# Kernel optimization log

Measured on AMD Instinct MI355X. Metric: run time of the kernel, lower is better.

## Reference

```python
import jax, jax.numpy as jnp
import numpy as np

BS, NA, NE, NAL = 128, 16, 16, 15
OWN, ALD, END = 30, 10, 10
H, HD, HYP, NACT = 64, 4, 64, 22
OUT_E = ((END + 1) * H + 1) * HD  # hyper_enemy output dim (weights + unused bias part)
OUT_A = ALD * H * HD


def setup_inputs() -> dict:
    key = jax.random.key(0)
    ks = jax.random.split(key, 30)
    s = 0.05
    r = lambda i, shape: jax.random.normal(ks[i], shape, dtype=jnp.float32) * s
    return {
        'bs': BS,
        'own_feats': r(0, (BS * NA, OWN)),
        'ally_feats': r(1, (BS * NA * NAL, ALD)),
        'enemy_feats': r(2, (BS * NA * NE, END)),
        'hidden_state': r(3, (BS * NA, H)),
        'fc1_w': r(4, (OWN, H)), 'fc1_b': r(5, (H,)),
        'he_w1': r(6, (END, HYP)), 'he_b1': r(7, (HYP,)),
        'he_w2': r(8, (HYP, OUT_E)), 'he_b2': r(9, (OUT_E,)),
        'ha_w1': r(10, (ALD, HYP)), 'ha_b1': r(11, (HYP,)),
        'ha_w2': r(12, (HYP, OUT_A)), 'ha_b2': r(13, (OUT_A,)),
        'merger_w': jnp.ones((1, HD, H), dtype=jnp.float32),
        'gru_wih': r(14, (3 * H, H)), 'gru_whh': r(15, (3 * H, H)),
        'gru_bih': r(16, (3 * H,)), 'gru_bhh': r(17, (3 * H,)),
        'fc2_w1': r(18, (H, H)), 'fc2_b1': r(19, (H,)),
        'fc2_w2': r(20, (H, NACT - 3)), 'fc2_b2': r(21, (NACT - 3,)),
        'pass_w1': r(22, (H, H)), 'pass_b1': r(23, (H,)),
        'pass_w2': r(24, (H, 3)), 'pass_b2': r(25, (3,)),
    }


def reference(bs, own_feats, ally_feats, enemy_feats, hidden_state,
              fc1_w, fc1_b, he_w1, he_b1, he_w2, he_b2,
              ha_w1, ha_b1, ha_w2, ha_b2, merger_w,
              gru_wih, gru_whh, gru_bih, gru_bhh,
              fc2_w1, fc2_b1, fc2_w2, fc2_b2,
              pass_w1, pass_b1, pass_w2, pass_b2):
    # own embedding: [bs*NA, H]
    emb_own = own_feats @ fc1_w + fc1_b

    # hypernet-generated enemy weights, consumed once then summed over enemies
    he = jax.nn.relu(enemy_feats @ he_w1 + he_b1) @ he_w2 + he_b2  # [bs*NA*NE, OUT_E]
    w_en = he[:, :END * H * HD].reshape(-1, END, H * HD)
    emb_en = jnp.einsum('ri,rio->ro', enemy_feats, w_en)
    emb_en = emb_en.reshape(bs * NA, NE, HD, H).sum(axis=1)  # [bs*NA, HD, H]

    ha = jax.nn.relu(ally_feats @ ha_w1 + ha_b1) @ ha_w2 + ha_b2  # [bs*NA*NAL, OUT_A]
    w_al = ha.reshape(-1, ALD, H * HD)
    emb_al4 = jnp.einsum('ri,rio->ro', ally_feats, w_al).reshape(bs * NA, NAL, HD, H)

    # passing_mlp -> [bs*NA, NAL, HD, 3]; permute/mean over heads, max over allies
    p = jax.nn.relu(emb_al4 @ pass_w1 + pass_b1) @ pass_w2 + pass_b2
    passing_dim = jnp.transpose(p, (0, 1, 3, 2)).mean(axis=-1)  # [bs*NA, NAL, 3]
    passing_embed = passing_dim.max(axis=1)  # [bs*NA, 3]

    emb_al = emb_al4.sum(axis=1)  # [bs*NA, HD, H]

    # Merger over heads
    mw = jax.nn.softmax(merger_w, axis=1)  # [1, HD, H]
    merged = jnp.sum(mw * (emb_en + emb_al), axis=1)  # [bs*NA, H]

    x = jax.nn.relu(emb_own + merged)

    # GRUCell (torch gate order: r, z, n)
    h_in = hidden_state.reshape(-1, H)
    gi = x @ gru_wih.T + gru_bih
    gh = h_in @ gru_whh.T + gru_bhh
    ir, iz, inn = jnp.split(gi, 3, axis=-1)
    hr, hz, hn = jnp.split(gh, 3, axis=-1)
    rg = jax.nn.sigmoid(ir + hr)
    zg = jax.nn.sigmoid(iz + hz)
    ng = jnp.tanh(inn + rg * hn)
    hh = (1.0 - zg) * ng + zg * h_in

    q_normal = (jax.nn.relu(hh @ fc2_w1 + fc2_b1) @ fc2_w2 + fc2_b2).reshape(bs, NA, -1)
    pe = passing_embed.reshape(bs, NA, 3)
    q = jnp.concatenate([q_normal[:, :, :9], pe, q_normal[:, :, 9:]], axis=-1)
    return q.reshape(bs, NA, -1), hh.reshape(bs, NA, -1)
```

## Files before the change

### kernel.cpp

```cpp
#include <hip/hip_runtime.h>
#include <hip/hip_bf16.h>

#define RAG   2048
#define KP2   704
#define QOFF  45056

typedef __attribute__((ext_vector_type(8))) short short8;
typedef __attribute__((ext_vector_type(4))) float f32x4;

__device__ inline unsigned short f2bf(float f){
    unsigned u = __float_as_uint(f);
    u += 0x7fffu + ((u >> 16) & 1u);
    return (unsigned short)(u >> 16);
}
__device__ inline unsigned pack2(float a, float b){
    return (unsigned)f2bf(a) | ((unsigned)f2bf(b) << 16);
}
__device__ inline void gload_lds(const void* g, void* l){
    __builtin_amdgcn_global_load_lds(
        (const __attribute__((address_space(1))) void*)g,
        (__attribute__((address_space(3))) void*)l, 16, 0, 0);
}

__global__ void __launch_bounds__(256) k_usum(
    const float* __restrict__ ef, const float* __restrict__ hew1, const float* __restrict__ heb1,
    const float* __restrict__ af, const float* __restrict__ haw1, const float* __restrict__ hab1,
    const float* __restrict__ hew2, const float* __restrict__ heb2,
    const float* __restrict__ haw2, const float* __restrict__ hab2,
    const float* __restrict__ wih, const float* __restrict__ whh, const float* __restrict__ f2w1,
    unsigned short* __restrict__ Bte, unsigned short* __restrict__ Bta,
    unsigned short* __restrict__ Wgru, unsigned short* __restrict__ B2,
    unsigned short* __restrict__ ha1, unsigned short* __restrict__ usum)
{
    int bb = blockIdx.x, tid = threadIdx.x;
    if (bb >= RAG){
        int p = bb - RAG;
        if (p < 22){
            int mat = p & 1;
            int s   = p >> 1;
            const float* w2 = mat ? haw2 : hew2;
            const float* b2 = mat ? hab2 : heb2;
            int ld = mat ? 2560 : 2820;
            unsigned short* Bt = mat ? Bta : Bte;
            int n = tid, n7 = n & 7;
            unsigned pk[32];
#pragma unroll
            for (int u2 = 0; u2 < 32; ++u2){
                int cst = u2 >> 2;
                int co  = cst ^ n7;
                int j0  = (u2 * 2) & 7;
                int k0 = s*64 + co*8 + j0, k1 = k0 + 1;
                float v0 = 0.f, v1 = 0.f;
                if (k0 < 640)      v0 = w2[(k0 & 63)*ld + (k0 >> 6)*256 + n];
                else if (k0 < 650) v0 = b2[(k0 - 640)*256 + n];
                if (k1 < 640)      v1 = w2[(k1 & 63)*ld + (k1 >> 6)*256 + n];
                else if (k1 < 650) v1 = b2[(k1 - 640)*256 + n];
                pk[u2] = pack2(v0, v1);
            }
            uint4* dst = (uint4*)&Bt[s*16384 + n*64];
#pragma unroll
            for (int q = 0; q < 8; ++q)
                dst[q] = (uint4){pk[q*4], pk[q*4+1], pk[q*4+2], pk[q*4+3]};
        } else if (p < 38){
            int base = (p - 22) * 2048;
#pragma unroll
            for (int i = 0; i < 8; ++i){
                int it = base + i*256 + tid;
                int n = it >> 7, k = it & 127;
                float v;
                if (n < 128)      v = (k < 64) ? wih[n*64 + k] : whh[n*64 + k - 64];
                else if (n < 192) v = (k < 64) ? wih[n*64 + k] : 0.f;
                else              v = (k < 64) ? 0.f : whh[(n-64)*64 + k - 64];
                Wgru[it] = f2bf(v);
            }
        } else {
            int base = (p - 38) * 2048;
#pragma unroll
            for (int i = 0; i < 8; ++i){
                int it = base + i*256 + tid;
                int n = it >> 6, k = it & 63;
                B2[it] = f2bf(f2w1[k*64 + n]);
            }
        }
        return;
    }
    __shared__ float s_ef[16][10], s_af[15][10];
    __shared__ float s_he[16][64], s_ha[15][64];
    int ag = bb;
    if (tid < 160) s_ef[tid/10][tid%10] = ef[ag*160 + tid];
    if (tid < 150) s_af[tid/10][tid%10] = af[ag*150 + tid];
    __syncthreads();
    for (int idx = tid; idx < 16*64; idx += 256){
        int en = idx >> 6, h = idx & 63;
        float s = heb1[h];
#pragma unroll
        for (int i = 0; i < 10; ++i) s = fmaf(s_ef[en][i], hew1[i*64 + h], s);
        s_he[en][h] = fmaxf(s, 0.f);
    }
    for (int idx = tid; idx < 15*64; idx += 256){
        int l = idx >> 6, h = idx & 63;
        float s = hab1[h];
#pragma unroll
        for (int i = 0; i < 10; ++i) s = fmaf(s_af[l][i], haw1[i*64 + h], s);
        s_ha[l][h] = fmaxf(s, 0.f);
    }
    __syncthreads();
    for (int idx = tid; idx < 15*64; idx += 256){
        int l = idx >> 6, h = idx & 63;
        ha1[(ag*15 + l)*64 + h] = f2bf(s_ha[l][h]);
    }
    for (int k = tid; k < KP2; k += 256){
        float ue = 0.f, ua = 0.f;
        if (k < 640){
            int i = k >> 6, h = k & 63;
#pragma unroll
            for (int en = 0; en < 16; ++en) ue = fmaf(s_he[en][h], s_ef[en][i], ue);
#pragma unroll
            for (int l = 0; l < 15; ++l) ua = fmaf(s_ha[l][h], s_af[l][i], ua);
        } else if (k < 650){
            int i = k - 640;
#pragma unroll
            for (int en = 0; en < 16; ++en) ue += s_ef[en][i];
#pragma unroll
            for (int l = 0; l < 15; ++l) ua += s_af[l][i];
        }
        usum[ag*KP2 + k]         = f2bf(ue);
        usum[(RAG + ag)*KP2 + k] = f2bf(ua);
    }
}

#define MFMA_STEP()                                                              \
    _Pragma("unroll")                                                            \
    for (int kk = 0; kk < 2; ++kk){                                              \
        int ch = ((kk*4 + quad) ^ l7) * 8;                                       \
        short8 a_[4], b_[4];                                                     \
        _Pragma("unroll")                                                        \
        for (int mt = 0; mt < 4; ++mt) a_[mt] = *(const short8*)&sA[(mt*16 + l15)*64 + ch]; \
        _Pragma("unroll")                                                        \
        for (int nt = 0; nt < 4; ++nt) b_[nt] = *(const short8*)&sB[(w*64 + nt*16 + l15)*64 + ch]; \
        _Pragma("unroll")                                                        \
        for (int mt = 0; mt < 4; ++mt)                                           \
        _Pragma("unroll")                                                        \
        for (int nt = 0; nt < 4; ++nt)                                           \
            acc[mt][nt] = __builtin_amdgcn_mfma_f32_16x16x32_bf16(a_[mt], b_[nt], acc[mt][nt], 0, 0, 0); \
    }

__global__ void __launch_bounds__(256, 2) k_gemm(
    const unsigned short* __restrict__ Bte, const unsigned short* __restrict__ Bta,
    const unsigned short* __restrict__ ha1, const float* __restrict__ af,
    const unsigned short* __restrict__ usum,
    const float* __restrict__ pw1, const float* __restrict__ pb1,
    const float* __restrict__ pw2, const float* __restrict__ pb2,
    float* __restrict__ emb, float* __restrict__ p2)
{
    __shared__ __align__(16) char smem[50176];
    unsigned short* sB  = (unsigned short*)smem;
    unsigned short* sA  = (unsigned short*)(smem + 32768);
    unsigned short* sW1 = (unsigned short*)(smem + 40960);

    int tid = threadIdx.x;
    int w = tid >> 6, lane = tid & 63;
    int l15 = lane & 15, quad = lane >> 4, l7 = l15 & 7;
    int bb = blockIdx.x;

    f32x4 acc[4][4];
#pragma unroll
    for (int a = 0; a < 4; ++a)
#pragma unroll
    for (int b = 0; b < 4; ++b) acc[a][b] = (f32x4){0.f, 0.f, 0.f, 0.f};

    if (bb < 480){
        int row0 = bb * 64;
        int r = tid >> 2, c4 = tid & 3, r7 = r & 7;
#pragma unroll
        for (int p = 0; p < 16; ++p){
            int idx = tid + p*256;
            sW1[(idx & 63)*72 + (idx >> 6)] = f2bf(pw1[idx]);
        }
        float af_reg[10];
        {
            const float* ap = af + (row0 + r)*10;
#pragma unroll
            for (int i = 0; i < 10; ++i) af_reg[i] = ap[i];
        }
        float h1f[16];
        {
            const unsigned short* hp = ha1 + (size_t)(row0 + r)*64 + c4*16;
            uint4 ra = *(const uint4*)hp;
            uint4 rb = *(const uint4*)(hp + 8);
            unsigned va[4] = {ra.x, ra.y, ra.z, ra.w};
            unsigned vb[4] = {rb.x, rb.y, rb.z, rb.w};
#pragma unroll
            for (int q = 0; q < 4; ++q){
                h1f[q*2+0]   = __uint_as_float(va[q] << 16);
                h1f[q*2+1]   = __uint_as_float(va[q] & 0xffff0000u);
                h1f[8+q*2+0] = __uint_as_float(vb[q] << 16);
                h1f[8+q*2+1] = __uint_as_float(vb[q] & 0xffff0000u);
            }
        }
        unsigned short* sAw0 = &sA[r*64 + (((2*c4)     ^ r7) * 8)];
        unsigned short* sAw1 = &sA[r*64 + (((2*c4 + 1) ^ r7) * 8)];
        const char* Bb = (const char*)Bta;
#pragma unroll
        for (int s = 0; s < 10; ++s){
            __syncthreads();
            const char* Bstep = Bb + s*32768;
#pragma unroll
            for (int ii = 0; ii < 8; ++ii)
                gload_lds(Bstep + w*8192 + ii*1024 + lane*16, smem + w*8192 + ii*1024);
            float avf = af_reg[s];
            uint4 p0, p1;
            p0.x = pack2(h1f[0]*avf,  h1f[1]*avf);  p0.y = pack2(h1f[2]*avf,  h1f[3]*avf);
            p0.z = pack2(h1f[4]*avf,  h1f[5]*avf);  p0.w = pack2(h1f[6]*avf,  h1f[7]*avf);
            p1.x = pack2(h1f[8]*avf,  h1f[9]*avf);  p1.y = pack2(h1f[10]*avf, h1f[11]*avf);
            p1.z = pack2(h1f[12]*avf, h1f[13]*avf); p1.w = pack2(h1f[14]*avf, h1f[15]*avf);
            *(uint4*)sAw0 = p0;
            *(uint4*)sAw1 = p1;
            __syncthreads();
            MFMA_STEP()
        }
        {
            __syncthreads();
            const char* Bstep = Bb + 10*32768;
#pragma unroll
            for (int ii = 0; ii < 8; ++ii)
                gload_lds(Bstep + w*8192 + ii*1024 + lane*16, smem + w*8192 + ii*1024);
            uint4 p0 = (uint4){0,0,0,0}, p1 = (uint4){0,0,0,0};
            if (c4 == 0){
                p0.x = pack2(af_reg[0], af_reg[1]); p0.y = pack2(af_reg[2], af_reg[3]);
                p0.z = pack2(af_reg[4], af_reg[5]); p0.w = pack2(af_reg[6], af_reg[7]);
                p1.x = pack2(af_reg[8], af_reg[9]);
            }
            *(uint4*)sAw0 = p0;
            *(uint4*)sAw1 = p1;
            __syncthreads();
            MFMA_STEP()
        }
        __syncthreads();
        unsigned short* sE = (unsigned short*)(smem + w*9216);
#pragma unroll
        for (int mt = 0; mt < 4; ++mt)
#pragma unroll
        for (int nt = 0; nt < 4; ++nt)
#pragma unroll
        for (int rg = 0; rg < 4; ++rg)
            sE[(mt*16 + quad*4 + rg)*72 + nt*16 + l15] = f2bf(acc[mt][nt][rg]);
        __syncthreads();
        f32x4 yacc[4][4];
#pragma unroll
        for (int a = 0; a < 4; ++a)
#pragma unroll
        for (int b = 0; b < 4; ++b) yacc[a][b] = (f32x4){0.f, 0.f, 0.f, 0.f};
#pragma unroll
        for (int kb = 0; kb < 2; ++kb){
            short8 ea[4], wb[4];
#pragma unroll
            for (int mt = 0; mt < 4; ++mt) ea[mt] = *(const short8*)&sE[(mt*16 + l15)*72 + kb*32 + quad*8];
#pragma unroll
            for (int ot = 0; ot < 4; ++ot) wb[ot] = *(const short8*)&sW1[(ot*16 + l15)*72 + kb*32 + quad*8];
#pragma unroll
            for (int mt = 0; mt < 4; ++mt)
#pragma unroll
            for (int ot = 0; ot < 4; ++ot)
                yacc[mt][ot] = __builtin_amdgcn_mfma_f32_16x16x32_bf16(ea[mt], wb[ot], yacc[mt][ot], 0, 0, 0);
        }
        float pb1v[4], w2r[4][3];
#pragma unroll
        for (int ot = 0; ot < 4; ++ot){
            pb1v[ot] = pb1[ot*16 + l15];
#pragma unroll
            for (int j = 0; j < 3; ++j) w2r[ot][j] = pw2[(ot*16 + l15)*3 + j];
        }
#pragma unroll
        for (int mt = 0; mt < 4; ++mt){
            float part[4][3];
#pragma unroll
            for (int rg = 0; rg < 4; ++rg)
#pragma unroll
            for (int j = 0; j < 3; ++j) part[rg][j] = 0.f;
#pragma unroll
            for (int ot = 0; ot < 4; ++ot)
#pragma unroll
            for (int rg = 0; rg < 4; ++rg){
                float yv = fmaxf(yacc[mt][ot][rg] + pb1v[ot], 0.f);
#pragma unroll
                for (int j = 0; j < 3; ++j) part[rg][j] = fmaf(yv, w2r[ot][j], part[rg][j]);
            }
#pragma unroll
            for (int off = 1; off < 16; off <<= 1)
#pragma unroll
            for (int rg = 0; rg < 4; ++rg)
#pragma unroll
            for (int j = 0; j < 3; ++j) part[rg][j] += __shfl_xor(part[rg][j], off, 64);
            if (l15 == 0){
#pragma unroll
                for (int rg = 0; rg < 4; ++rg)
#pragma unroll
                for (int j = 0; j < 3; ++j)
                    p2[(row0 + mt*16 + quad*4 + rg)*12 + w*3 + j] = part[rg][j] + pb2[j];
            }
        }
    } else {
        int row0 = (bb - 480) * 64;
        const char* Bb = (const char*)((row0 < RAG) ? Bte : Bta);
        const char* Ub = (const char*)usum;
        int corig = (lane & 7) ^ (lane >> 3);
        size_t aoff = (size_t)(row0 + w*16 + (lane >> 3)) * (KP2*2) + corig*16;
#pragma unroll
        for (int s = 0; s < 11; ++s){
            __syncthreads();
            const char* Bstep = Bb + s*32768;
#pragma unroll
            for (int ii = 0; ii < 8; ++ii)
                gload_lds(Bstep + w*8192 + ii*1024 + lane*16, smem + w*8192 + ii*1024);
            gload_lds(Ub + aoff + s*128,              smem + 32768 + w*2048);
            gload_lds(Ub + aoff + 8*(KP2*2) + s*128,  smem + 32768 + w*2048 + 1024);
            __syncthreads();
            MFMA_STEP()
        }
#pragma unroll
        for (int mt = 0; mt < 4; ++mt)
#pragma unroll
        for (int nt = 0; nt < 4; ++nt)
#pragma unroll
        for (int rg = 0; rg < 4; ++rg)
            emb[(row0 + mt*16 + quad*4 + rg)*256 + w*64 + nt*16 + l15] = acc[mt][nt][rg];
    }
}

__global__ void __launch_bounds__(256) k_final(
    const float* __restrict__ own, const float* __restrict__ hidden,
    const float* __restrict__ fc1w, const float* __restrict__ fc1b,
    const float* __restrict__ mergw,
    const float* __restrict__ bih, const float* __restrict__ bhh,
    const float* __restrict__ f2b1, const float* __restrict__ f2w2, const float* __restrict__ f2b2,
    const unsigned short* __restrict__ Wgru, const unsigned short* __restrict__ B2,
    const float* __restrict__ emb, const float* __restrict__ p2,
    float* __restrict__ out)
{
    __shared__ __align__(16) unsigned short sA16[16*128];
    __shared__ float sHin[16*65];
    __shared__ float sG[256*17];
    __shared__ float sH2f[16*65];
    __shared__ __align__(16) unsigned short sH2b[16*64];
    __shared__ float sY[16*68];

    int tid = threadIdx.x;
    int w = tid >> 6, lane = tid & 63;
    int l15 = lane & 15, quad = lane >> 4;
    int ag0 = blockIdx.x * 16;

#pragma unroll
    for (int p = 0; p < 4; ++p){
        int idx = tid + p*256;
        int h = idx & 63, a = idx >> 6;
        int ag = ag0 + a;
        float s = fc1b[h];
        const float* ow = own + ag*30;
#pragma unroll
        for (int c = 0; c < 30; ++c) s = fmaf(ow[c], fc1w[c*64 + h], s);
        float m0 = mergw[h], m1 = mergw[64+h], m2 = mergw[128+h], m3 = mergw[192+h];
        float mx = fmaxf(fmaxf(m0, m1), fmaxf(m2, m3));
        float e0 = __expf(m0-mx), e1 = __expf(m1-mx), e2 = __expf(m2-mx), e3 = __expf(m3-mx);
        float inv = 1.f / (e0+e1+e2+e3);
        const float* een = emb + ag*256;
        const float* eal = emb + (RAG + ag)*256;
        float mg = (e0*(een[h]+eal[h]) + e1*(een[64+h]+eal[64+h]) +
                    e2*(een[128+h]+eal[128+h]) + e3*(een[192+h]+eal[192+h])) * inv;
        float x = fmaxf(s + mg, 0.f);
        float hin = hidden[ag*64 + h];
        sA16[a*128 + h]      = f2bf(x);
        sA16[a*128 + 64 + h] = f2bf(hin);
        sHin[a*65 + h] = hin;
    }
    __syncthreads();
    {
        f32x4 g_[4];
#pragma unroll
        for (int t = 0; t < 4; ++t) g_[t] = (f32x4){0.f,0.f,0.f,0.f};
#pragma unroll
        for (int ks = 0; ks < 4; ++ks){
            int kt = ks*32;
            short8 a8 = *(const short8*)&sA16[l15*128 + kt + quad*8];
#pragma unroll
            for (int t = 0; t < 4; ++t){
                int col = (w*4 + t)*16 + l15;
                short8 b8 = *(const short8*)&Wgru[col*128 + kt + quad*8];
                g_[t] = __builtin_amdgcn_mfma_f32_16x16x32_bf16(a8, b8, g_[t], 0, 0, 0);
            }
        }
#pragma unroll
        for (int t = 0; t < 4; ++t){
            int col = (w*4 + t)*16 + l15;
#pragma unroll
            for (int rg = 0; rg < 4; ++rg) sG[col*17 + quad*4 + rg] = g_[t][rg];
        }
    }
    __syncthreads();
#pragma unroll
    for (int p = 0; p < 4; ++p){
        int idx = tid + p*256;
        int a = idx & 15, h = idx >> 4;
        float rs  = sG[h*17 + a]        + bih[h]      + bhh[h];
        float zs  = sG[(64+h)*17 + a]   + bih[64+h]   + bhh[64+h];
        float in_ = sG[(128+h)*17 + a]  + bih[128+h];
        float hn  = sG[(192+h)*17 + a]  + bhh[128+h];
        float r = 1.f / (1.f + __expf(-rs));
        float z = 1.f / (1.f + __expf(-zs));
        float n = tanhf(in_ + r*hn);
        float hv = (1.f - z)*n + z*sHin[a*65 + h];
        sH2f[a*65 + h] = hv;
        sH2b[a*64 + h] = f2bf(hv);
    }
    __syncthreads();
    {
        f32x4 y = (f32x4){0.f,0.f,0.f,0.f};
#pragma unroll
        for (int ks = 0; ks < 2; ++ks){
            int kt = ks*32;
            short8 a8 = *(const short8*)&sH2b[l15*64 + kt + quad*8];
            short8 b8 = *(const short8*)&B2[(w*16 + l15)*64 + kt + quad*8];
            y = __builtin_amdgcn_mfma_f32_16x16x32_bf16(a8, b8, y, 0, 0, 0);
        }
        float b1v = f2b1[w*16 + l15];
#pragma unroll
        for (int rg = 0; rg < 4; ++rg)
            sY[(quad*4 + rg)*68 + w*16 + l15] = fmaxf(y[rg] + b1v, 0.f);
    }
    __syncthreads();
    for (int idx = tid; idx < 16*19; idx += 256){
        int a = idx / 19, j = idx - a*19;
        float s2 = f2b2[j];
        for (int c = 0; c < 64; ++c) s2 = fmaf(sY[a*68 + c], f2w2[c*19 + j], s2);
        out[(ag0 + a)*22 + ((j < 9) ? j : j + 3)] = s2;
    }
    if (tid < 48){
        int a = tid / 3, j = tid - a*3;
        float best = -1e30f;
        const float* pp = p2 + (ag0 + a)*180;
        for (int l = 0; l < 15; ++l){
            float mean = 0.25f*(pp[l*12 + j] + pp[l*12 + 3 + j] + pp[l*12 + 6 + j] + pp[l*12 + 9 + j]);
            best = fmaxf(best, mean);
        }
        out[(ag0 + a)*22 + 9 + j] = best;
    }
#pragma unroll
    for (int p = 0; p < 4; ++p){
        int idx = tid + p*256;
        int h = idx & 63, a = idx >> 6;
        out[QOFF + (ag0 + a)*64 + h] = sH2f[a*65 + h];
    }
}

extern "C" void kernel_launch(void* const* d_in, const int* in_sizes, int n_in,
                              void* d_out, int out_size, void* d_ws, size_t ws_size,
                              hipStream_t stream) {
    const float* own    = (const float*)d_in[1];
    const float* allyf  = (const float*)d_in[2];
    const float* enemyf = (const float*)d_in[3];
    const float* hidden = (const float*)d_in[4];
    const float* fc1w   = (const float*)d_in[5];
    const float* fc1b   = (const float*)d_in[6];
    const float* hew1   = (const float*)d_in[7];
    const float* heb1   = (const float*)d_in[8];
    const float* hew2   = (const float*)d_in[9];
    const float* heb2   = (const float*)d_in[10];
    const float* haw1   = (const float*)d_in[11];
    const float* hab1   = (const float*)d_in[12];
    const float* haw2   = (const float*)d_in[13];
    const float* hab2   = (const float*)d_in[14];
    const float* mergw  = (const float*)d_in[15];
    const float* wih    = (const float*)d_in[16];
    const float* whh    = (const float*)d_in[17];
    const float* bih    = (const float*)d_in[18];
    const float* bhh    = (const float*)d_in[19];
    const float* f2w1   = (const float*)d_in[20];
    const float* f2b1   = (const float*)d_in[21];
    const float* f2w2   = (const float*)d_in[22];
    const float* f2b2   = (const float*)d_in[23];
    const float* pw1    = (const float*)d_in[24];
    const float* pb1    = (const float*)d_in[25];
    const float* pw2    = (const float*)d_in[26];
    const float* pb2    = (const float*)d_in[27];
    float* out = (float*)d_out;

    char* W = (char*)d_ws;
    unsigned short* Bte  = (unsigned short*)(W + 0);
    unsigned short* Bta  = (unsigned short*)(W + 360448);
    unsigned short* usum = (unsigned short*)(W + 720896);
    float*          emb  = (float*)(W + 6488064);
    float*          p2   = (float*)(W + 10682368);
    unsigned short* ha1  = (unsigned short*)(W + 12156928);
    unsigned short* Wgru = (unsigned short*)(W + 16089088);
    unsigned short* B2   = (unsigned short*)(W + 16154624);

    k_usum<<<RAG + 40, 256, 0, stream>>>(enemyf, hew1, heb1, allyf, haw1, hab1,
                                         hew2, heb2, haw2, hab2, wih, whh, f2w1,
                                         Bte, Bta, Wgru, B2, ha1, usum);
    k_gemm<<<544, 256, 0, stream>>>(Bte, Bta, ha1, allyf, usum,
                                    pw1, pb1, pw2, pb2, emb, p2);
    k_final<<<RAG/16, 256, 0, stream>>>(own, hidden, fc1w, fc1b, mergw,
                                        bih, bhh, f2b1, f2w2, f2b2,
                                        Wgru, B2, emb, p2, out);
}
```

Baseline: 187.3 us.

## Double GEMM row tile to 128 rows per block to reuse B tiles

```diff
diff --git a/kernel.cpp b/kernel.cpp
--- a/kernel.cpp
+++ b/kernel.cpp
@@ -129,17 +129,17 @@
     }
 }
 
-#define MFMA_STEP()                                                              \
+#define MFMA_STEP8()                                                             \
     _Pragma("unroll")                                                            \
     for (int kk = 0; kk < 2; ++kk){                                              \
         int ch = ((kk*4 + quad) ^ l7) * 8;                                       \
-        short8 a_[4], b_[4];                                                     \
+        short8 a_[8], b_[4];                                                     \
         _Pragma("unroll")                                                        \
-        for (int mt = 0; mt < 4; ++mt) a_[mt] = *(const short8*)&sA[(mt*16 + l15)*64 + ch]; \
+        for (int mt = 0; mt < 8; ++mt) a_[mt] = *(const short8*)&sA[(mt*16 + l15)*64 + ch]; \
         _Pragma("unroll")                                                        \
         for (int nt = 0; nt < 4; ++nt) b_[nt] = *(const short8*)&sB[(w*64 + nt*16 + l15)*64 + ch]; \
         _Pragma("unroll")                                                        \
-        for (int mt = 0; mt < 4; ++mt)                                           \
+        for (int mt = 0; mt < 8; ++mt)                                           \
         _Pragma("unroll")                                                        \
         for (int nt = 0; nt < 4; ++nt)                                           \
             acc[mt][nt] = __builtin_amdgcn_mfma_f32_16x16x32_bf16(a_[mt], b_[nt], acc[mt][nt], 0, 0, 0); \
@@ -153,25 +153,25 @@
     const float* __restrict__ pw2, const float* __restrict__ pb2,
     float* __restrict__ emb, float* __restrict__ p2)
 {
-    __shared__ __align__(16) char smem[50176];
+    __shared__ __align__(16) char smem[58368];
     unsigned short* sB  = (unsigned short*)smem;
     unsigned short* sA  = (unsigned short*)(smem + 32768);
-    unsigned short* sW1 = (unsigned short*)(smem + 40960);
+    unsigned short* sW1 = (unsigned short*)(smem + 49152);
 
     int tid = threadIdx.x;
     int w = tid >> 6, lane = tid & 63;
     int l15 = lane & 15, quad = lane >> 4, l7 = l15 & 7;
     int bb = blockIdx.x;
 
-    f32x4 acc[4][4];
-#pragma unroll
-    for (int a = 0; a < 4; ++a)
+    f32x4 acc[8][4];
+#pragma unroll
+    for (int a = 0; a < 8; ++a)
 #pragma unroll
     for (int b = 0; b < 4; ++b) acc[a][b] = (f32x4){0.f, 0.f, 0.f, 0.f};
 
-    if (bb < 480){
-        int row0 = bb * 64;
-        int r = tid >> 2, c4 = tid & 3, r7 = r & 7;
+    if (bb < 240){
+        int row0 = bb * 128;
+        int r = tid >> 1, half = tid & 1, r7 = r & 7;
 #pragma unroll
         for (int p = 0; p < 16; ++p){
             int idx = tid + p*256;
@@ -183,23 +183,24 @@
 #pragma unroll
             for (int i = 0; i < 10; ++i) af_reg[i] = ap[i];
         }
-        float h1f[16];
+        float h1f[32];
         {
-            const unsigned short* hp = ha1 + (size_t)(row0 + r)*64 + c4*16;
-            uint4 ra = *(const uint4*)hp;
-            uint4 rb = *(const uint4*)(hp + 8);
-            unsigned va[4] = {ra.x, ra.y, ra.z, ra.w};
-            unsigned vb[4] = {rb.x, rb.y, rb.z, rb.w};
-#pragma unroll
-            for (int q = 0; q < 4; ++q){
-                h1f[q*2+0]   = __uint_as_float(va[q] << 16);
-                h1f[q*2+1]   = __uint_as_float(va[q] & 0xffff0000u);
-                h1f[8+q*2+0] = __uint_as_float(vb[q] << 16);
-                h1f[8+q*2+1] = __uint_as_float(vb[q] & 0xffff0000u);
-            }
-        }
-        unsigned short* sAw0 = &sA[r*64 + (((2*c4)     ^ r7) * 8)];
-        unsigned short* sAw1 = &sA[r*64 + (((2*c4 + 1) ^ r7) * 8)];
+            const unsigned short* hp = ha1 + (size_t)(row0 + r)*64 + half*32;
+#pragma unroll
+            for (int m = 0; m < 4; ++m){
+                uint4 u = *(const uint4*)(hp + m*8);
+                unsigned uu[4] = {u.x, u.y, u.z, u.w};
+#pragma unroll
+                for (int q = 0; q < 4; ++q){
+                    h1f[m*8 + q*2 + 0] = __uint_as_float(uu[q] << 16);
+                    h1f[m*8 + q*2 + 1] = __uint_as_float(uu[q] & 0xffff0000u);
+                }
+            }
+        }
+        unsigned short* sAw[4];
+#pragma unroll
+        for (int q = 0; q < 4; ++q)
+            sAw[q] = &sA[r*64 + (((half*4 + q) ^ r7) * 8)];
         const char* Bb = (const char*)Bta;
 #pragma unroll
         for (int s = 0; s < 10; ++s){
@@ -209,15 +210,17 @@
             for (int ii = 0; ii < 8; ++ii)
                 gload_lds(Bstep + w*8192 + ii*1024 + lane*16, smem + w*8192 + ii*1024);
             float avf = af_reg[s];
-            uint4 p0, p1;
-            p0.x = pack2(h1f[0]*avf,  h1f[1]*avf);  p0.y = pack2(h1f[2]*avf,  h1f[3]*avf);
-            p0.z = pack2(h1f[4]*avf,  h1f[5]*avf);  p0.w = pack2(h1f[6]*avf,  h1f[7]*avf);
-            p1.x = pack2(h1f[8]*avf,  h1f[9]*avf);  p1.y = pack2(h1f[10]*avf, h1f[11]*avf);
-            p1.z = pack2(h1f[12]*avf, h1f[13]*avf); p1.w = pack2(h1f[14]*avf, h1f[15]*avf);
-            *(uint4*)sAw0 = p0;
-            *(uint4*)sAw1 = p1;
-            __syncthreads();
-            MFMA_STEP()
+#pragma unroll
+            for (int q = 0; q < 4; ++q){
+                uint4 pv;
+                pv.x = pack2(h1f[q*8+0]*avf, h1f[q*8+1]*avf);
+                pv.y = pack2(h1f[q*8+2]*avf, h1f[q*8+3]*avf);
+                pv.z = pack2(h1f[q*8+4]*avf, h1f[q*8+5]*avf);
+                pv.w = pack2(h1f[q*8+6]*avf, h1f[q*8+7]*avf);
+                *(uint4*)sAw[q] = pv;
+            }
+            __syncthreads();
+            MFMA_STEP8()
         }
         {
             __syncthreads();
@@ -225,44 +228,18 @@
 #pragma unroll
             for (int ii = 0; ii < 8; ++ii)
                 gload_lds(Bstep + w*8192 + ii*1024 + lane*16, smem + w*8192 + ii*1024);
-            uint4 p0 = (uint4){0,0,0,0}, p1 = (uint4){0,0,0,0};
-            if (c4 == 0){
-                p0.x = pack2(af_reg[0], af_reg[1]); p0.y = pack2(af_reg[2], af_reg[3]);
-                p0.z = pack2(af_reg[4], af_reg[5]); p0.w = pack2(af_reg[6], af_reg[7]);
-                p1.x = pack2(af_reg[8], af_reg[9]);
-            }
-            *(uint4*)sAw0 = p0;
-            *(uint4*)sAw1 = p1;
-            __syncthreads();
-            MFMA_STEP()
-        }
-        __syncthreads();
-        unsigned short* sE = (unsigned short*)(smem + w*9216);
-#pragma unroll
-        for (int mt = 0; mt < 4; ++mt)
-#pragma unroll
-        for (int nt = 0; nt < 4; ++nt)
-#pragma unroll
-        for (int rg = 0; rg < 4; ++rg)
-            sE[(mt*16 + quad*4 + rg)*72 + nt*16 + l15] = f2bf(acc[mt][nt][rg]);
-        __syncthreads();
-        f32x4 yacc[4][4];
-#pragma unroll
-        for (int a = 0; a < 4; ++a)
-#pragma unroll
-        for (int b = 0; b < 4; ++b) yacc[a][b] = (f32x4){0.f, 0.f, 0.f, 0.f};
-#pragma unroll
-        for (int kb = 0; kb < 2; ++kb){
-            short8 ea[4], wb[4];
-#pragma unroll
-            for (int mt = 0; mt < 4; ++mt) ea[mt] = *(const short8*)&sE[(mt*16 + l15)*72 + kb*32 + quad*8];
-#pragma unroll
-            for (int ot = 0; ot < 4; ++ot) wb[ot] = *(const short8*)&sW1[(ot*16 + l15)*72 + kb*32 + quad*8];
-#pragma unroll
-            for (int mt = 0; mt < 4; ++mt)
-#pragma unroll
-            for (int ot = 0; ot < 4; ++ot)
-                yacc[mt][ot] = __builtin_amdgcn_mfma_f32_16x16x32_bf16(ea[mt], wb[ot], yacc[mt][ot], 0, 0, 0);
+            uint4 pv[4];
+#pragma unroll
+            for (int q = 0; q < 4; ++q) pv[q] = (uint4){0,0,0,0};
+            if (half == 0){
+                pv[0].x = pack2(af_reg[0], af_reg[1]); pv[0].y = pack2(af_reg[2], af_reg[3]);
+                pv[0].z = pack2(af_reg[4], af_reg[5]); pv[0].w = pack2(af_reg[6], af_reg[7]);
+                pv[1].x = pack2(af_reg[8], af_reg[9]);
+            }
+#pragma unroll
+            for (int q = 0; q < 4; ++q) *(uint4*)sAw[q] = pv[q];
+            __syncthreads();
+            MFMA_STEP8()
         }
         float pb1v[4], w2r[4][3];
 #pragma unroll
@@ -271,41 +248,72 @@
 #pragma unroll
             for (int j = 0; j < 3; ++j) w2r[ot][j] = pw2[(ot*16 + l15)*3 + j];
         }
-#pragma unroll
-        for (int mt = 0; mt < 4; ++mt){
-            float part[4][3];
+        unsigned short* sE = (unsigned short*)(smem + w*9216);
+#pragma unroll
+        for (int ps = 0; ps < 2; ++ps){
+            __syncthreads();
+#pragma unroll
+            for (int mt = 0; mt < 4; ++mt)
+#pragma unroll
+            for (int nt = 0; nt < 4; ++nt)
 #pragma unroll
             for (int rg = 0; rg < 4; ++rg)
-#pragma unroll
-            for (int j = 0; j < 3; ++j) part[rg][j] = 0.f;
-#pragma unroll
-            for (int ot = 0; ot < 4; ++ot)
-#pragma unroll
-            for (int rg = 0; rg < 4; ++rg){
-                float yv = fmaxf(yacc[mt][ot][rg] + pb1v[ot], 0.f);
-#pragma unroll
-                for (int j = 0; j < 3; ++j) part[rg][j] = fmaf(yv, w2r[ot][j], part[rg][j]);
-            }
-#pragma unroll
-            for (int off = 1; off < 16; off <<= 1)
-#pragma unroll
-            for (int rg = 0; rg < 4; ++rg)
-#pragma unroll
-            for (int j = 0; j < 3; ++j) part[rg][j] += __shfl_xor(part[rg][j], off, 64);
-            if (l15 == 0){
+                sE[(mt*16 + quad*4 + rg)*72 + nt*16 + l15] = f2bf(acc[ps*4 + mt][nt][rg]);
+            __syncthreads();
+            f32x4 yacc[4][4];
+#pragma unroll
+            for (int a = 0; a < 4; ++a)
+#pragma unroll
+            for (int b = 0; b < 4; ++b) yacc[a][b] = (f32x4){0.f, 0.f, 0.f, 0.f};
+#pragma unroll
+            for (int kb = 0; kb < 2; ++kb){
+                short8 ea[4], wb[4];
+#pragma unroll
+                for (int mt = 0; mt < 4; ++mt) ea[mt] = *(const short8*)&sE[(mt*16 + l15)*72 + kb*32 + quad*8];
+#pragma unroll
+                for (int ot = 0; ot < 4; ++ot) wb[ot] = *(const short8*)&sW1[(ot*16 + l15)*72 + kb*32 + quad*8];
+#pragma unroll
+                for (int mt = 0; mt < 4; ++mt)
+#pragma unroll
+                for (int ot = 0; ot < 4; ++ot)
+                    yacc[mt][ot] = __builtin_amdgcn_mfma_f32_16x16x32_bf16(ea[mt], wb[ot], yacc[mt][ot], 0, 0, 0);
+            }
+#pragma unroll
+            for (int mt = 0; mt < 4; ++mt){
+                float part[4][3];
 #pragma unroll
                 for (int rg = 0; rg < 4; ++rg)
 #pragma unroll
-                for (int j = 0; j < 3; ++j)
-                    p2[(row0 + mt*16 + quad*4 + rg)*12 + w*3 + j] = part[rg][j] + pb2[j];
+                for (int j = 0; j < 3; ++j) part[rg][j] = 0.f;
+#pragma unroll
+                for (int ot = 0; ot < 4; ++ot)
+#pragma unroll
+                for (int rg = 0; rg < 4; ++rg){
+                    float yv = fmaxf(yacc[mt][ot][rg] + pb1v[ot], 0.f);
+#pragma unroll
+                    for (int j = 0; j < 3; ++j) part[rg][j] = fmaf(yv, w2r[ot][j], part[rg][j]);
+                }
+#pragma unroll
+                for (int off = 1; off < 16; off <<= 1)
+#pragma unroll
+                for (int rg = 0; rg < 4; ++rg)
+#pragma unroll
+                for (int j = 0; j < 3; ++j) part[rg][j] += __shfl_xor(part[rg][j], off, 64);
+                if (l15 == 0){
+#pragma unroll
+                    for (int rg = 0; rg < 4; ++rg)
+#pragma unroll
+                    for (int j = 0; j < 3; ++j)
+                        p2[(row0 + ps*64 + mt*16 + quad*4 + rg)*12 + w*3 + j] = part[rg][j] + pb2[j];
+                }
             }
         }
     } else {
-        int row0 = (bb - 480) * 64;
+        int row0 = (bb - 240) * 128;
         const char* Bb = (const char*)((row0 < RAG) ? Bte : Bta);
         const char* Ub = (const char*)usum;
         int corig = (lane & 7) ^ (lane >> 3);
-        size_t aoff = (size_t)(row0 + w*16 + (lane >> 3)) * (KP2*2) + corig*16;
+        size_t abase = (size_t)(row0 + w*32 + (lane >> 3)) * (KP2*2) + corig*16;
 #pragma unroll
         for (int s = 0; s < 11; ++s){
             __syncthreads();
@@ -313,13 +321,15 @@
 #pragma unroll
             for (int ii = 0; ii < 8; ++ii)
                 gload_lds(Bstep + w*8192 + ii*1024 + lane*16, smem + w*8192 + ii*1024);
-            gload_lds(Ub + aoff + s*128,              smem + 32768 + w*2048);
-            gload_lds(Ub + aoff + 8*(KP2*2) + s*128,  smem + 32768 + w*2048 + 1024);
-            __syncthreads();
-            MFMA_STEP()
-        }
-#pragma unroll
-        for (int mt = 0; mt < 4; ++mt)
+#pragma unroll
+            for (int ii = 0; ii < 4; ++ii)
+                gload_lds(Ub + abase + (size_t)ii*8*(KP2*2) + s*128,
+                          smem + 32768 + w*4096 + ii*1024);
+            __syncthreads();
+            MFMA_STEP8()
+        }
+#pragma unroll
+        for (int mt = 0; mt < 8; ++mt)
 #pragma unroll
         for (int nt = 0; nt < 4; ++nt)
 #pragma unroll
@@ -497,7 +507,7 @@
     k_usum<<<RAG + 40, 256, 0, stream>>>(enemyf, hew1, heb1, allyf, haw1, hab1,
                                          hew2, heb2, haw2, hab2, wih, whh, f2w1,
                                          Bte, Bta, Wgru, B2, ha1, usum);
-    k_gemm<<<544, 256, 0, stream>>>(Bte, Bta, ha1, allyf, usum,
+    k_gemm<<<272, 256, 0, stream>>>(Bte, Bta, ha1, allyf, usum,
                                     pw1, pb1, pw2, pb2, emb, p2);
     k_final<<<RAG/16, 256, 0, stream>>>(own, hidden, fc1w, fc1b, mergw,
                                         bih, bhh, f2b1, f2w2, f2b2,
```

After: 189.0 us. About the same (+0.9%).

## Split k_gemm output columns across two blocks to double grid and occupancy

Applied to the files above, without the earlier changes.

```diff
diff --git a/kernel.cpp b/kernel.cpp
--- a/kernel.cpp
+++ b/kernel.cpp
@@ -129,23 +129,23 @@
     }
 }
 
-#define MFMA_STEP()                                                              \
+#define MFMA_STEP42()                                                            \
     _Pragma("unroll")                                                            \
     for (int kk = 0; kk < 2; ++kk){                                              \
         int ch = ((kk*4 + quad) ^ l7) * 8;                                       \
-        short8 a_[4], b_[4];                                                     \
+        short8 a_[4], b_[2];                                                     \
         _Pragma("unroll")                                                        \
         for (int mt = 0; mt < 4; ++mt) a_[mt] = *(const short8*)&sA[(mt*16 + l15)*64 + ch]; \
         _Pragma("unroll")                                                        \
-        for (int nt = 0; nt < 4; ++nt) b_[nt] = *(const short8*)&sB[(w*64 + nt*16 + l15)*64 + ch]; \
+        for (int nt = 0; nt < 2; ++nt) b_[nt] = *(const short8*)&sB[(w*32 + nt*16 + l15)*64 + ch]; \
         _Pragma("unroll")                                                        \
         for (int mt = 0; mt < 4; ++mt)                                           \
         _Pragma("unroll")                                                        \
-        for (int nt = 0; nt < 4; ++nt)                                           \
+        for (int nt = 0; nt < 2; ++nt)                                           \
             acc[mt][nt] = __builtin_amdgcn_mfma_f32_16x16x32_bf16(a_[mt], b_[nt], acc[mt][nt], 0, 0, 0); \
     }
 
-__global__ void __launch_bounds__(256, 2) k_gemm(
+__global__ void __launch_bounds__(256, 4) k_gemm(
     const unsigned short* __restrict__ Bte, const unsigned short* __restrict__ Bta,
     const unsigned short* __restrict__ ha1, const float* __restrict__ af,
     const unsigned short* __restrict__ usum,
@@ -153,30 +153,25 @@
     const float* __restrict__ pw2, const float* __restrict__ pb2,
     float* __restrict__ emb, float* __restrict__ p2)
 {
-    __shared__ __align__(16) char smem[50176];
-    unsigned short* sB  = (unsigned short*)smem;
-    unsigned short* sA  = (unsigned short*)(smem + 32768);
-    unsigned short* sW1 = (unsigned short*)(smem + 40960);
+    __shared__ __align__(16) char smem[33792];
+    unsigned short* sB = (unsigned short*)smem;
+    unsigned short* sA = (unsigned short*)(smem + 16384);
 
     int tid = threadIdx.x;
     int w = tid >> 6, lane = tid & 63;
     int l15 = lane & 15, quad = lane >> 4, l7 = l15 & 7;
     int bb = blockIdx.x;
 
-    f32x4 acc[4][4];
+    f32x4 acc[4][2];
 #pragma unroll
     for (int a = 0; a < 4; ++a)
 #pragma unroll
-    for (int b = 0; b < 4; ++b) acc[a][b] = (f32x4){0.f, 0.f, 0.f, 0.f};
-
-    if (bb < 480){
-        int row0 = bb * 64;
+    for (int b = 0; b < 2; ++b) acc[a][b] = (f32x4){0.f, 0.f, 0.f, 0.f};
+
+    if (bb < 960){
+        int rt = bb >> 1, c = bb & 1;
+        int row0 = rt * 64;
         int r = tid >> 2, c4 = tid & 3, r7 = r & 7;
-#pragma unroll
-        for (int p = 0; p < 16; ++p){
-            int idx = tid + p*256;
-            sW1[(idx & 63)*72 + (idx >> 6)] = f2bf(pw1[idx]);
-        }
         float af_reg[10];
         {
             const float* ap = af + (row0 + r)*10;
@@ -204,10 +199,10 @@
 #pragma unroll
         for (int s = 0; s < 10; ++s){
             __syncthreads();
-            const char* Bstep = Bb + s*32768;
-#pragma unroll
-            for (int ii = 0; ii < 8; ++ii)
-                gload_lds(Bstep + w*8192 + ii*1024 + lane*16, smem + w*8192 + ii*1024);
+            const char* Bstep = Bb + s*32768 + c*16384;
+#pragma unroll
+            for (int ii = 0; ii < 4; ++ii)
+                gload_lds(Bstep + w*4096 + ii*1024 + lane*16, smem + w*4096 + ii*1024);
             float avf = af_reg[s];
             uint4 p0, p1;
             p0.x = pack2(h1f[0]*avf,  h1f[1]*avf);  p0.y = pack2(h1f[2]*avf,  h1f[3]*avf);
@@ -217,14 +212,14 @@
             *(uint4*)sAw0 = p0;
             *(uint4*)sAw1 = p1;
             __syncthreads();
-            MFMA_STEP()
+            MFMA_STEP42()
         }
         {
             __syncthreads();
-            const char* Bstep = Bb + 10*32768;
-#pragma unroll
-            for (int ii = 0; ii < 8; ++ii)
-                gload_lds(Bstep + w*8192 + ii*1024 + lane*16, smem + w*8192 + ii*1024);
+            const char* Bstep = Bb + 10*32768 + c*16384;
+#pragma unroll
+            for (int ii = 0; ii < 4; ++ii)
+                gload_lds(Bstep + w*4096 + ii*1024 + lane*16, smem + w*4096 + ii*1024);
             uint4 p0 = (uint4){0,0,0,0}, p1 = (uint4){0,0,0,0};
             if (c4 == 0){
                 p0.x = pack2(af_reg[0], af_reg[1]); p0.y = pack2(af_reg[2], af_reg[3]);
@@ -234,42 +229,50 @@
             *(uint4*)sAw0 = p0;
             *(uint4*)sAw1 = p1;
             __syncthreads();
-            MFMA_STEP()
+            MFMA_STEP42()
         }
         __syncthreads();
-        unsigned short* sE = (unsigned short*)(smem + w*9216);
+        unsigned short* sW1 = (unsigned short*)smem;
+        unsigned short* sE  = (unsigned short*)(smem + 9216 + (w >> 1)*9216);
+        float* sP = (float*)(smem + 27648);
+#pragma unroll
+        for (int p = 0; p < 16; ++p){
+            int idx = tid + p*256;
+            sW1[(idx & 63)*72 + (idx >> 6)] = f2bf(pw1[idx]);
+        }
 #pragma unroll
         for (int mt = 0; mt < 4; ++mt)
 #pragma unroll
-        for (int nt = 0; nt < 4; ++nt)
+        for (int nt = 0; nt < 2; ++nt)
 #pragma unroll
         for (int rg = 0; rg < 4; ++rg)
-            sE[(mt*16 + quad*4 + rg)*72 + nt*16 + l15] = f2bf(acc[mt][nt][rg]);
+            sE[(mt*16 + quad*4 + rg)*72 + (w & 1)*32 + nt*16 + l15] = f2bf(acc[mt][nt][rg]);
         __syncthreads();
-        f32x4 yacc[4][4];
+        f32x4 yacc[4][2];
 #pragma unroll
         for (int a = 0; a < 4; ++a)
 #pragma unroll
-        for (int b = 0; b < 4; ++b) yacc[a][b] = (f32x4){0.f, 0.f, 0.f, 0.f};
+        for (int b = 0; b < 2; ++b) yacc[a][b] = (f32x4){0.f, 0.f, 0.f, 0.f};
 #pragma unroll
         for (int kb = 0; kb < 2; ++kb){
-            short8 ea[4], wb[4];
+            short8 ea[4], wb[2];
 #pragma unroll
             for (int mt = 0; mt < 4; ++mt) ea[mt] = *(const short8*)&sE[(mt*16 + l15)*72 + kb*32 + quad*8];
 #pragma unroll
-            for (int ot = 0; ot < 4; ++ot) wb[ot] = *(const short8*)&sW1[(ot*16 + l15)*72 + kb*32 + quad*8];
+            for (int ot = 0; ot < 2; ++ot) wb[ot] = *(const short8*)&sW1[((w & 1)*32 + ot*16 + l15)*72 + kb*32 + quad*8];
 #pragma unroll
             for (int mt = 0; mt < 4; ++mt)
 #pragma unroll
-            for (int ot = 0; ot < 4; ++ot)
+            for (int ot = 0; ot < 2; ++ot)
                 yacc[mt][ot] = __builtin_amdgcn_mfma_f32_16x16x32_bf16(ea[mt], wb[ot], yacc[mt][ot], 0, 0, 0);
         }
-        float pb1v[4], w2r[4][3];
-#pragma unroll
-        for (int ot = 0; ot < 4; ++ot){
-            pb1v[ot] = pb1[ot*16 + l15];
-#pragma unroll
-            for (int j = 0; j < 3; ++j) w2r[ot][j] = pw2[(ot*16 + l15)*3 + j];
+        float pb1v[2], w2r[2][3];
+#pragma unroll
+        for (int ot = 0; ot < 2; ++ot){
+            int hc = (w & 1)*32 + ot*16 + l15;
+            pb1v[ot] = pb1[hc];
+#pragma unroll
+            for (int j = 0; j < 3; ++j) w2r[ot][j] = pw2[hc*3 + j];
         }
 #pragma unroll
         for (int mt = 0; mt < 4; ++mt){
@@ -279,7 +282,7 @@
 #pragma unroll
             for (int j = 0; j < 3; ++j) part[rg][j] = 0.f;
 #pragma unroll
-            for (int ot = 0; ot < 4; ++ot)
+            for (int ot = 0; ot < 2; ++ot)
 #pragma unroll
             for (int rg = 0; rg < 4; ++rg){
                 float yv = fmaxf(yacc[mt][ot][rg] + pb1v[ot], 0.f);
@@ -297,34 +300,45 @@
                 for (int rg = 0; rg < 4; ++rg)
 #pragma unroll
                 for (int j = 0; j < 3; ++j)
-                    p2[(row0 + mt*16 + quad*4 + rg)*12 + w*3 + j] = part[rg][j] + pb2[j];
-            }
+                    sP[(((w >> 1)*2 + (w & 1))*64 + mt*16 + quad*4 + rg)*3 + j] = part[rg][j];
+            }
+        }
+        __syncthreads();
+        for (int idx = tid; idx < 384; idx += 256){
+            int hh = idx / 192, rem = idx - hh*192;
+            int rr = rem / 3, j = rem - rr*3;
+            float v = sP[((hh*2 + 0)*64 + rr)*3 + j] + sP[((hh*2 + 1)*64 + rr)*3 + j] + pb2[j];
+            p2[(row0 + rr)*12 + (c*2 + hh)*3 + j] = v;
         }
     } else {
-        int row0 = (bb - 480) * 64;
+        int e = bb - 960;
+        int rt = e >> 1, c = e & 1;
+        int row0 = rt * 64;
         const char* Bb = (const char*)((row0 < RAG) ? Bte : Bta);
         const char* Ub = (const char*)usum;
-        int corig = (lane & 7) ^ (lane >> 3);
-        size_t aoff = (size_t)(row0 + w*16 + (lane >> 3)) * (KP2*2) + corig*16;
+        int co = (lane & 7) ^ (lane >> 3);
+        size_t abase = (size_t)(row0 + w*16 + (lane >> 3)) * (KP2*2) + co*16;
 #pragma unroll
         for (int s = 0; s < 11; ++s){
             __syncthreads();
-            const char* Bstep = Bb + s*32768;
-#pragma unroll
-            for (int ii = 0; ii < 8; ++ii)
-                gload_lds(Bstep + w*8192 + ii*1024 + lane*16, smem + w*8192 + ii*1024);
-            gload_lds(Ub + aoff + s*128,              smem + 32768 + w*2048);
-            gload_lds(Ub + aoff + 8*(KP2*2) + s*128,  smem + 32768 + w*2048 + 1024);
+            const char* Bstep = Bb + s*32768 + c*16384;
+#pragma unroll
+            for (int ii = 0; ii < 4; ++ii)
+                gload_lds(Bstep + w*4096 + ii*1024 + lane*16, smem + w*4096 + ii*1024);
+#pragma unroll
+            for (int ii = 0; ii < 2; ++ii)
+                gload_lds(Ub + abase + (size_t)ii*8*(KP2*2) + s*128,
+                          smem + 16384 + w*2048 + ii*1024);
             __syncthreads();
-            MFMA_STEP()
+            MFMA_STEP42()
         }
 #pragma unroll
         for (int mt = 0; mt < 4; ++mt)
 #pragma unroll
-        for (int nt = 0; nt < 4; ++nt)
+        for (int nt = 0; nt < 2; ++nt)
 #pragma unroll
         for (int rg = 0; rg < 4; ++rg)
-            emb[(row0 + mt*16 + quad*4 + rg)*256 + w*64 + nt*16 + l15] = acc[mt][nt][rg];
+            emb[(row0 + mt*16 + quad*4 + rg)*256 + c*128 + w*32 + nt*16 + l15] = acc[mt][nt][rg];
     }
 }
 
@@ -497,8 +511,8 @@
     k_usum<<<RAG + 40, 256, 0, stream>>>(enemyf, hew1, heb1, allyf, haw1, hab1,
                                          hew2, heb2, haw2, hab2, wih, whh, f2w1,
                                          Bte, Bta, Wgru, B2, ha1, usum);
-    k_gemm<<<544, 256, 0, stream>>>(Bte, Bta, ha1, allyf, usum,
-                                    pw1, pb1, pw2, pb2, emb, p2);
+    k_gemm<<<1088, 256, 0, stream>>>(Bte, Bta, ha1, allyf, usum,
+                                     pw1, pb1, pw2, pb2, emb, p2);
     k_final<<<RAG/16, 256, 0, stream>>>(own, hidden, fc1w, fc1b, mergw,
                                         bih, bhh, f2b1, f2w2, f2b2,
                                         Wgru, B2, emb, p2, out);
```

Result: no change. 190.9 us (+1.9%).
